# Performance work log

Hardware: AMD Instinct MI355X
Metric: run time of the kernel (lower is better)

Reference implementation:

```python
import jax, jax.numpy as jnp
import numpy as np

NUM_DIM = 1024
NUM_HEAD = 4


def setup_inputs() -> dict:
    key = jax.random.key(0)
    k1, k2, k3, k4, k5, k6 = jax.random.split(key, 6)
    B, N, C = 8, 2048, NUM_DIM
    x = jax.random.normal(k1, (B, N, C), dtype=jnp.float32)
    tmp_token = jax.random.normal(k2, (1, 1, C), dtype=jnp.float32)
    s = 1.0 / np.sqrt(C)
    Wqkv = jax.random.uniform(k3, (C, 3 * C), dtype=jnp.float32, minval=-s, maxval=s)
    bqkv = jax.random.uniform(k4, (3 * C,), dtype=jnp.float32, minval=-s, maxval=s)
    # Note: original module zero-inits v_proj; we use random weights for a
    # non-degenerate correctness baseline.
    Wv = jax.random.uniform(k5, (C, C), dtype=jnp.float32, minval=-s, maxval=s)
    bv = jax.random.uniform(k6, (C,), dtype=jnp.float32, minval=-s, maxval=s)
    return {"input": x, "tmp_token": tmp_token, "Wqkv": Wqkv, "bqkv": bqkv, "Wv": Wv, "bv": bv}


def reference(input, tmp_token, Wqkv, bqkv, Wv, bv):
    B = input.shape[0]
    # prepend learned token -> [B, N+1, C]
    x = jnp.concatenate([jnp.broadcast_to(tmp_token, (B, 1, tmp_token.shape[-1])), input], axis=1)
    B, N, C = x.shape
    H, Dh = NUM_HEAD, C // NUM_HEAD
    qkv = (x @ Wqkv + bqkv).reshape(B, N, 3, H, Dh)
    q = qkv[:, :, 0].transpose(0, 2, 1, 3)  # [B, H, N, Dh]
    k = qkv[:, :, 1].transpose(0, 2, 1, 3)
    v = qkv[:, :, 2].transpose(0, 2, 1, 3)
    scale = Dh ** (-0.5)
    scores = jnp.einsum("bhqd,bhkd->bhqk", q, k) * scale
    att = jax.nn.softmax(scores, axis=-1)  # dropout is identity in eval mode
    out = jnp.einsum("bhqk,bhkd->bhqd", att, v)
    out = out.transpose(0, 2, 1, 3).reshape(B, N, C)
    out = out @ Wv + bv  # op dropout identity in eval
    return out[:, 0, :]
```

## Files before the change

kernel.cpp:

```cpp
#include <hip/hip_runtime.h>
#include <math.h>

#define CDIM 1024
#define TC   3072
#define NIN  2048

#define OFF_Q0P 0
#define OFF_WS  16384
#define OFF_PS  20480
#define OFF_PY  24576
#define OFF_YB  2121728
#define OFF_OCP 2154496

__global__ void k_q0(const float* __restrict__ t, const float* __restrict__ W,
                     float* __restrict__ wsb) {
    int ic = blockIdx.x >> 3, jc = blockIdx.x & 7;
    int j = jc * 128 + threadIdx.x;
    int i0 = ic * 64;
    float acc = 0.f;
    for (int i = 0; i < 64; ++i)
        acc += t[i0 + i] * W[(size_t)(i0 + i) * TC + j];
    wsb[OFF_Q0P + ic * CDIM + j] = acc;
}

__global__ void k_ws(const float* __restrict__ W, const float* __restrict__ bqkv,
                     float* __restrict__ wsb) {
    int wave = threadIdx.x >> 6, lane = threadIdx.x & 63;
    int c = blockIdx.x, h = wave;
    int d0 = h * 256 + lane * 4;
    float4 wv = *(const float4*)&W[(size_t)c * TC + CDIM + d0];
    float4 q = *(const float4*)&bqkv[d0];
#pragma unroll
    for (int ic = 0; ic < 16; ++ic) {
        float4 p = *(const float4*)&wsb[OFF_Q0P + ic * CDIM + d0];
        q.x += p.x; q.y += p.y; q.z += p.z; q.w += p.w;
    }
    float acc = wv.x * q.x + wv.y * q.y + wv.z * q.z + wv.w * q.w;
    for (int off = 32; off > 0; off >>= 1) acc += __shfl_down(acc, off);
    if (lane == 0) wsb[OFF_WS + h * CDIM + c] = acc;
}

__global__ __launch_bounds__(256) void k_pass1(const float* __restrict__ x,
                                               float* __restrict__ wsb) {
    int tid = threadIdx.x, lane = tid & 63, wave = tid >> 6;
    int b = blockIdx.x >> 6, blkc = blockIdx.x & 63;

    float4 wsr[4][4];
#pragma unroll
    for (int k = 0; k < 4; ++k)
#pragma unroll
        for (int h = 0; h < 4; ++h)
            wsr[k][h] = *(const float4*)&wsb[OFF_WS + h * CDIM + k * 256 + lane * 4];

    float s[4] = {0.f, 0.f, 0.f, 0.f};
    float4 y[4][4];
#pragma unroll
    for (int h = 0; h < 4; ++h)
#pragma unroll
        for (int k = 0; k < 4; ++k) y[h][k] = make_float4(0.f, 0.f, 0.f, 0.f);

    const float* base = x + ((size_t)b * NIN + blkc * 32 + wave * 8) * CDIM;
#pragma unroll 4
    for (int i = 0; i < 8; ++i) {
        const float* row = base + (size_t)i * CDIM;
        float4 xv[4];
#pragma unroll
        for (int k = 0; k < 4; ++k) xv[k] = *(const float4*)&row[k * 256 + lane * 4];
        float e[4];
#pragma unroll
        for (int h = 0; h < 4; ++h) {
            float a = 0.f;
#pragma unroll
            for (int k = 0; k < 4; ++k)
                a += xv[k].x * wsr[k][h].x + xv[k].y * wsr[k][h].y +
                     xv[k].z * wsr[k][h].z + xv[k].w * wsr[k][h].w;
            for (int off = 1; off < 64; off <<= 1) a += __shfl_xor(a, off);
            e[h] = __expf(a * 0.0625f);
        }
#pragma unroll
        for (int h = 0; h < 4; ++h) {
            float f = e[h];
            s[h] += f;
#pragma unroll
            for (int k = 0; k < 4; ++k) {
                y[h][k].x += f * xv[k].x; y[h][k].y += f * xv[k].y;
                y[h][k].z += f * xv[k].z; y[h][k].w += f * xv[k].w;
            }
        }
    }

    __shared__ float ss[4][4];
    __shared__ float ybuf[4][CDIM];
    if (lane == 0)
#pragma unroll
        for (int h = 0; h < 4; ++h) ss[wave][h] = s[h];
    for (int idx = tid; idx < 4 * CDIM; idx += 256) ((float*)ybuf)[idx] = 0.f;
    __syncthreads();
    for (int w = 0; w < 4; ++w) {
        if (wave == w) {
#pragma unroll
            for (int h = 0; h < 4; ++h)
#pragma unroll
                for (int k = 0; k < 4; ++k) {
                    float4* dst = (float4*)&ybuf[h][k * 256 + lane * 4];
                    float4 v = *dst;
                    v.x += y[h][k].x; v.y += y[h][k].y;
                    v.z += y[h][k].z; v.w += y[h][k].w;
                    *dst = v;
                }
        }
        __syncthreads();
    }
    int p = blockIdx.x;
    if (tid < 4)
        wsb[OFF_PS + p * 4 + tid] = ss[0][tid] + ss[1][tid] + ss[2][tid] + ss[3][tid];
    for (int idx = tid; idx < 4 * CDIM; idx += 256)
        wsb[OFF_PY + (size_t)p * 4096 + idx] = ((float*)ybuf)[idx];
}

__global__ void k_comb(const float* __restrict__ t, float* __restrict__ wsb) {
    int tid = threadIdx.x, lane = tid & 63, wv = tid >> 6;
    int blk = blockIdx.x;
    int b = blk >> 4, h = (blk >> 2) & 3, cq = blk & 3;
    __shared__ float red[4], redS[4];

    int c0 = tid * 4;
    float4 tv = *(const float4*)&t[c0];
    float4 wsv = *(const float4*)&wsb[OFF_WS + h * CDIM + c0];
    float p = tv.x * wsv.x + tv.y * wsv.y + tv.z * wsv.z + tv.w * wsv.w;
    for (int off = 1; off < 64; off <<= 1) p += __shfl_xor(p, off);
    if (lane == 0) red[wv] = p;

    float sv = (tid < 64) ? wsb[OFF_PS + (size_t)(b * 64 + tid) * 4 + h] : 0.f;
    for (int off = 1; off < 64; off <<= 1) sv += __shfl_xor(sv, off);
    if (lane == 0) redS[wv] = sv;
    __syncthreads();
    float sc0 = (red[0] + red[1] + red[2] + red[3]) * 0.0625f;
    float e0 = __expf(sc0);
    float S = redS[0] + redS[1] + redS[2] + redS[3] + e0;

    int c = cq * 256 + tid;
    float acc = e0 * t[c];
#pragma unroll 4
    for (int j = 0; j < 64; ++j)
        acc += wsb[OFF_PY + (size_t)(b * 64 + j) * 4096 + h * CDIM + c];
    wsb[OFF_YB + (size_t)(b * 4 + h) * CDIM + c] = acc / S;
}

__global__ void k_ocy(const float* __restrict__ W, const float* __restrict__ bqkv,
                      float* __restrict__ wsb, float* __restrict__ out) {
    out[blockIdx.x * 128 + threadIdx.x] = 0.f;

    int p = blockIdx.x >> 3, q = blockIdx.x & 7;
    int h = p >> 1;
    __shared__ float sL[1024];
    for (int bb = 0; bb < 8; ++bb)
        sL[bb * 128 + threadIdx.x] = wsb[OFF_YB + (size_t)(bb * 4 + h) * CDIM + q * 128 + threadIdx.x];
    __syncthreads();
    int cp = p * 128 + threadIdx.x;
    float acc[8] = {0.f, 0.f, 0.f, 0.f, 0.f, 0.f, 0.f, 0.f};
    for (int c = 0; c < 128; ++c) {
        float wv = W[(size_t)(q * 128 + c) * TC + 2 * CDIM + cp];
#pragma unroll
        for (int bb = 0; bb < 8; ++bb) acc[bb] += sL[bb * 128 + c] * wv;
    }
    if (q == 0) {
        float bias = bqkv[2 * CDIM + cp];
#pragma unroll
        for (int bb = 0; bb < 8; ++bb) acc[bb] += bias;
    }
#pragma unroll
    for (int bb = 0; bb < 8; ++bb)
        wsb[OFF_OCP + (size_t)(q * 8 + bb) * CDIM + cp] = acc[bb];
}

__global__ void k_out(const float* __restrict__ Wv, const float* __restrict__ bv,
                      const float* __restrict__ wsb, float* __restrict__ out) {
    int jp = blockIdx.x >> 3, cq = blockIdx.x & 7;
    __shared__ float ocL[1024];
    for (int bb = 0; bb < 8; ++bb) {
        float sum = 0.f;
#pragma unroll
        for (int q = 0; q < 8; ++q)
            sum += wsb[OFF_OCP + (size_t)(q * 8 + bb) * CDIM + cq * 128 + threadIdx.x];
        ocL[bb * 128 + threadIdx.x] = sum;
    }
    __syncthreads();
    int j = jp * 128 + threadIdx.x;
    float acc[8] = {0.f, 0.f, 0.f, 0.f, 0.f, 0.f, 0.f, 0.f};
    for (int c = 0; c < 128; ++c) {
        float wv = Wv[(size_t)(cq * 128 + c) * CDIM + j];
#pragma unroll
        for (int bb = 0; bb < 8; ++bb) acc[bb] += ocL[bb * 128 + c] * wv;
    }
    if (cq == 0) {
        float bias = bv[j];
#pragma unroll
        for (int bb = 0; bb < 8; ++bb) acc[bb] += bias;
    }
#pragma unroll
    for (int bb = 0; bb < 8; ++bb) atomicAdd(&out[bb * CDIM + j], acc[bb]);
}

extern "C" void kernel_launch(void* const* d_in, const int* in_sizes, int n_in,
                              void* d_out, int out_size, void* d_ws, size_t ws_size,
                              hipStream_t stream) {
    const float* x    = (const float*)d_in[0];
    const float* t    = (const float*)d_in[1];
    const float* Wqkv = (const float*)d_in[2];
    const float* bqkv = (const float*)d_in[3];
    const float* Wv   = (const float*)d_in[4];
    const float* bv   = (const float*)d_in[5];
    float* wsb = (float*)d_ws;
    float* out = (float*)d_out;

    k_q0   <<<128,  128, 0, stream>>>(t, Wqkv, wsb);
    k_ws   <<<1024, 256, 0, stream>>>(Wqkv, bqkv, wsb);
    k_pass1<<<512,  256, 0, stream>>>(x, wsb);
    k_comb <<<128,  256, 0, stream>>>(t, wsb);
    k_ocy  <<<64,   128, 0, stream>>>(Wqkv, bqkv, wsb, out);
    k_out  <<<64,   128, 0, stream>>>(Wv, bv, wsb, out);
}
```

Baseline: 176.8 us.

## Fuse six kernels into one cooperative kernel with grid-wide syncs

Replaces six separate launches with one cooperative kernel of 256 blocks that separates its phases with grid.sync(). The work split is rebalanced: each block handles 64 rows of x instead of 32, which halves the partial-sum buffers. The last two GEMVs use split-K reductions in shared memory, which removes the zeroing of the output and the atomicAdd. This aims to cut launch overhead and inter-kernel gaps. The cost is grid-barrier overhead, and the x-streaming phase now runs on only 256 blocks, which may reduce memory parallelism.

```diff
diff --git a/kernel.cpp b/kernel.cpp
--- a/kernel.cpp
+++ b/kernel.cpp
@@ -1,5 +1,8 @@
 #include <hip/hip_runtime.h>
+#include <hip/hip_cooperative_groups.h>
 #include <math.h>
+
+namespace cg = cooperative_groups;
 
 #define CDIM 1024
 #define TC   3072
@@ -8,198 +11,212 @@
 #define OFF_Q0P 0
 #define OFF_WS  16384
 #define OFF_PS  20480
-#define OFF_PY  24576
-#define OFF_YB  2121728
-#define OFF_OCP 2154496
-
-__global__ void k_q0(const float* __restrict__ t, const float* __restrict__ W,
-                     float* __restrict__ wsb) {
-    int ic = blockIdx.x >> 3, jc = blockIdx.x & 7;
-    int j = jc * 128 + threadIdx.x;
-    int i0 = ic * 64;
-    float acc = 0.f;
-    for (int i = 0; i < 64; ++i)
-        acc += t[i0 + i] * W[(size_t)(i0 + i) * TC + j];
-    wsb[OFF_Q0P + ic * CDIM + j] = acc;
-}
-
-__global__ void k_ws(const float* __restrict__ W, const float* __restrict__ bqkv,
-                     float* __restrict__ wsb) {
-    int wave = threadIdx.x >> 6, lane = threadIdx.x & 63;
-    int c = blockIdx.x, h = wave;
-    int d0 = h * 256 + lane * 4;
-    float4 wv = *(const float4*)&W[(size_t)c * TC + CDIM + d0];
-    float4 q = *(const float4*)&bqkv[d0];
-#pragma unroll
-    for (int ic = 0; ic < 16; ++ic) {
-        float4 p = *(const float4*)&wsb[OFF_Q0P + ic * CDIM + d0];
-        q.x += p.x; q.y += p.y; q.z += p.z; q.w += p.w;
-    }
-    float acc = wv.x * q.x + wv.y * q.y + wv.z * q.z + wv.w * q.w;
-    for (int off = 32; off > 0; off >>= 1) acc += __shfl_down(acc, off);
-    if (lane == 0) wsb[OFF_WS + h * CDIM + c] = acc;
-}
-
-__global__ __launch_bounds__(256) void k_pass1(const float* __restrict__ x,
-                                               float* __restrict__ wsb) {
-    int tid = threadIdx.x, lane = tid & 63, wave = tid >> 6;
-    int b = blockIdx.x >> 6, blkc = blockIdx.x & 63;
-
-    float4 wsr[4][4];
-#pragma unroll
-    for (int k = 0; k < 4; ++k)
+#define OFF_PY  21504
+#define OFF_YB  1070080
+#define OFF_OC  1102848
+
+__global__ __launch_bounds__(256) void k_fused(
+    const float* __restrict__ x, const float* __restrict__ t,
+    const float* __restrict__ W, const float* __restrict__ bqkv,
+    const float* __restrict__ Wv, const float* __restrict__ bv,
+    float* __restrict__ wsb, float* __restrict__ out)
+{
+    cg::grid_group grid = cg::this_grid();
+    const int bid = blockIdx.x, tid = threadIdx.x;
+    const int lane = tid & 63, wave = tid >> 6;
+    __shared__ float lds[4112];
+
+    {
+        int ic = bid >> 4, jc = bid & 15;
+        int j = jc * 64 + lane;
+        int i0 = ic * 64 + wave * 16;
+        float acc = 0.f;
+#pragma unroll
+        for (int ii = 0; ii < 16; ++ii)
+            acc += t[i0 + ii] * W[(size_t)(i0 + ii) * TC + j];
+        lds[wave * 64 + lane] = acc;
+        __syncthreads();
+        if (wave == 0)
+            wsb[OFF_Q0P + ic * CDIM + j] =
+                lds[lane] + lds[64 + lane] + lds[128 + lane] + lds[192 + lane];
+    }
+    grid.sync();
+
+    {
+        for (int d = tid; d < CDIM; d += 256) {
+            float s = bqkv[d];
+#pragma unroll
+            for (int ic = 0; ic < 16; ++ic) s += wsb[OFF_Q0P + ic * CDIM + d];
+            lds[d] = s;
+        }
+        __syncthreads();
+        int c = bid * 4 + wave;
+        const float* wr = &W[(size_t)c * TC + CDIM];
+#pragma unroll
+        for (int h = 0; h < 4; ++h) {
+            float4 wv = *(const float4*)&wr[h * 256 + lane * 4];
+            float4 qv = *(const float4*)&lds[h * 256 + lane * 4];
+            float a = wv.x * qv.x + wv.y * qv.y + wv.z * qv.z + wv.w * qv.w;
+            for (int off = 32; off; off >>= 1) a += __shfl_down(a, off);
+            if (lane == 0) wsb[OFF_WS + h * CDIM + c] = a;
+        }
+    }
+    grid.sync();
+
+    {
+        int b = bid >> 5, blkc = bid & 31;
+        float4 wsr[4][4];
+#pragma unroll
+        for (int k = 0; k < 4; ++k)
+#pragma unroll
+            for (int h = 0; h < 4; ++h)
+                wsr[k][h] = *(const float4*)&wsb[OFF_WS + h * CDIM + k * 256 + lane * 4];
+
+        float s[4] = {0.f, 0.f, 0.f, 0.f};
+        float4 y[4][4];
 #pragma unroll
         for (int h = 0; h < 4; ++h)
-            wsr[k][h] = *(const float4*)&wsb[OFF_WS + h * CDIM + k * 256 + lane * 4];
-
-    float s[4] = {0.f, 0.f, 0.f, 0.f};
-    float4 y[4][4];
-#pragma unroll
-    for (int h = 0; h < 4; ++h)
-#pragma unroll
-        for (int k = 0; k < 4; ++k) y[h][k] = make_float4(0.f, 0.f, 0.f, 0.f);
-
-    const float* base = x + ((size_t)b * NIN + blkc * 32 + wave * 8) * CDIM;
-#pragma unroll 4
-    for (int i = 0; i < 8; ++i) {
-        const float* row = base + (size_t)i * CDIM;
-        float4 xv[4];
-#pragma unroll
-        for (int k = 0; k < 4; ++k) xv[k] = *(const float4*)&row[k * 256 + lane * 4];
-        float e[4];
-#pragma unroll
-        for (int h = 0; h < 4; ++h) {
+#pragma unroll
+            for (int k = 0; k < 4; ++k) y[h][k] = make_float4(0.f, 0.f, 0.f, 0.f);
+
+        const float* base = x + ((size_t)b * NIN + blkc * 64 + wave * 16) * CDIM;
+#pragma unroll 4
+        for (int i = 0; i < 16; ++i) {
+            const float* row = base + (size_t)i * CDIM;
+            float4 xv[4];
+#pragma unroll
+            for (int k = 0; k < 4; ++k) xv[k] = *(const float4*)&row[k * 256 + lane * 4];
+            float e[4];
+#pragma unroll
+            for (int h = 0; h < 4; ++h) {
+                float a = 0.f;
+#pragma unroll
+                for (int k = 0; k < 4; ++k)
+                    a += xv[k].x * wsr[k][h].x + xv[k].y * wsr[k][h].y +
+                         xv[k].z * wsr[k][h].z + xv[k].w * wsr[k][h].w;
+                for (int off = 1; off < 64; off <<= 1) a += __shfl_xor(a, off);
+                e[h] = __expf(a * 0.0625f);
+            }
+#pragma unroll
+            for (int h = 0; h < 4; ++h) {
+                float f = e[h];
+                s[h] += f;
+#pragma unroll
+                for (int k = 0; k < 4; ++k) {
+                    y[h][k].x += f * xv[k].x; y[h][k].y += f * xv[k].y;
+                    y[h][k].z += f * xv[k].z; y[h][k].w += f * xv[k].w;
+                }
+            }
+        }
+
+        if (lane == 0)
+#pragma unroll
+            for (int h = 0; h < 4; ++h) lds[4096 + wave * 4 + h] = s[h];
+        for (int idx = tid; idx < 4096; idx += 256) lds[idx] = 0.f;
+        __syncthreads();
+        for (int w = 0; w < 4; ++w) {
+            if (wave == w) {
+#pragma unroll
+                for (int h = 0; h < 4; ++h)
+#pragma unroll
+                    for (int k = 0; k < 4; ++k) {
+                        float4* dst = (float4*)&lds[h * CDIM + k * 256 + lane * 4];
+                        float4 v = *dst;
+                        v.x += y[h][k].x; v.y += y[h][k].y;
+                        v.z += y[h][k].z; v.w += y[h][k].w;
+                        *dst = v;
+                    }
+            }
+            __syncthreads();
+        }
+        if (tid < 4)
+            wsb[OFF_PS + bid * 4 + tid] =
+                lds[4096 + tid] + lds[4100 + tid] + lds[4104 + tid] + lds[4108 + tid];
+        for (int idx = tid; idx < 4096; idx += 256)
+            wsb[OFF_PY + (size_t)bid * 4096 + idx] = lds[idx];
+    }
+    grid.sync();
+
+    {
+        int b = bid >> 5, r = bid & 31, h = r >> 3, cq = r & 7;
+        float4 tv = *(const float4*)&t[tid * 4];
+        float4 wv = *(const float4*)&wsb[OFF_WS + h * CDIM + tid * 4];
+        float p = tv.x * wv.x + tv.y * wv.y + tv.z * wv.z + tv.w * wv.w;
+        for (int off = 1; off < 64; off <<= 1) p += __shfl_xor(p, off);
+        float sv = 0.f;
+        if (wave == 0) {
+            sv = (lane < 32) ? wsb[OFF_PS + (size_t)(b * 32 + lane) * 4 + h] : 0.f;
+            for (int off = 1; off < 64; off <<= 1) sv += __shfl_xor(sv, off);
+        }
+        if (lane == 0) lds[4096 + wave] = p;
+        if (tid == 0) lds[4100] = sv;
+        __syncthreads();
+        float sc0 = (lds[4096] + lds[4097] + lds[4098] + lds[4099]) * 0.0625f;
+        float e0 = __expf(sc0);
+        float S = lds[4100] + e0;
+
+        int c = cq * 128 + (tid & 127), half = tid >> 7;
+        float acc = 0.f;
+#pragma unroll 4
+        for (int jj = 0; jj < 16; ++jj)
+            acc += wsb[OFF_PY + (size_t)(b * 32 + half * 16 + jj) * 4096 + h * CDIM + c];
+        lds[half * 128 + (tid & 127)] = acc;
+        __syncthreads();
+        if (half == 0) {
+            float tot = lds[tid] + lds[128 + tid] + e0 * t[c];
+            wsb[OFF_YB + ((size_t)b * 4 + h) * CDIM + c] = tot / S;
+        }
+    }
+    grid.sync();
+
+    {
+        int b = bid & 7, jc = bid >> 3;
+        int hh = jc >> 3;
+        for (int d = tid; d < CDIM; d += 256)
+            lds[d] = wsb[OFF_YB + ((size_t)b * 4 + hh) * CDIM + d];
+        __syncthreads();
+        int cp = jc * 32 + (tid & 31), cs = tid >> 5;
+        const float* wcol = &W[2 * CDIM + cp];
+        float acc = 0.f;
+#pragma unroll 4
+        for (int cc = 0; cc < 128; ++cc) {
+            int c = cs * 128 + cc;
+            acc += lds[c] * wcol[(size_t)c * TC];
+        }
+        __syncthreads();
+        lds[cs * 32 + (tid & 31)] = acc;
+        __syncthreads();
+        if (cs == 0) {
             float a = 0.f;
 #pragma unroll
-            for (int k = 0; k < 4; ++k)
-                a += xv[k].x * wsr[k][h].x + xv[k].y * wsr[k][h].y +
-                     xv[k].z * wsr[k][h].z + xv[k].w * wsr[k][h].w;
-            for (int off = 1; off < 64; off <<= 1) a += __shfl_xor(a, off);
-            e[h] = __expf(a * 0.0625f);
-        }
-#pragma unroll
-        for (int h = 0; h < 4; ++h) {
-            float f = e[h];
-            s[h] += f;
-#pragma unroll
-            for (int k = 0; k < 4; ++k) {
-                y[h][k].x += f * xv[k].x; y[h][k].y += f * xv[k].y;
-                y[h][k].z += f * xv[k].z; y[h][k].w += f * xv[k].w;
-            }
-        }
-    }
-
-    __shared__ float ss[4][4];
-    __shared__ float ybuf[4][CDIM];
-    if (lane == 0)
-#pragma unroll
-        for (int h = 0; h < 4; ++h) ss[wave][h] = s[h];
-    for (int idx = tid; idx < 4 * CDIM; idx += 256) ((float*)ybuf)[idx] = 0.f;
-    __syncthreads();
-    for (int w = 0; w < 4; ++w) {
-        if (wave == w) {
-#pragma unroll
-            for (int h = 0; h < 4; ++h)
-#pragma unroll
-                for (int k = 0; k < 4; ++k) {
-                    float4* dst = (float4*)&ybuf[h][k * 256 + lane * 4];
-                    float4 v = *dst;
-                    v.x += y[h][k].x; v.y += y[h][k].y;
-                    v.z += y[h][k].z; v.w += y[h][k].w;
-                    *dst = v;
-                }
-        }
-        __syncthreads();
-    }
-    int p = blockIdx.x;
-    if (tid < 4)
-        wsb[OFF_PS + p * 4 + tid] = ss[0][tid] + ss[1][tid] + ss[2][tid] + ss[3][tid];
-    for (int idx = tid; idx < 4 * CDIM; idx += 256)
-        wsb[OFF_PY + (size_t)p * 4096 + idx] = ((float*)ybuf)[idx];
-}
-
-__global__ void k_comb(const float* __restrict__ t, float* __restrict__ wsb) {
-    int tid = threadIdx.x, lane = tid & 63, wv = tid >> 6;
-    int blk = blockIdx.x;
-    int b = blk >> 4, h = (blk >> 2) & 3, cq = blk & 3;
-    __shared__ float red[4], redS[4];
-
-    int c0 = tid * 4;
-    float4 tv = *(const float4*)&t[c0];
-    float4 wsv = *(const float4*)&wsb[OFF_WS + h * CDIM + c0];
-    float p = tv.x * wsv.x + tv.y * wsv.y + tv.z * wsv.z + tv.w * wsv.w;
-    for (int off = 1; off < 64; off <<= 1) p += __shfl_xor(p, off);
-    if (lane == 0) red[wv] = p;
-
-    float sv = (tid < 64) ? wsb[OFF_PS + (size_t)(b * 64 + tid) * 4 + h] : 0.f;
-    for (int off = 1; off < 64; off <<= 1) sv += __shfl_xor(sv, off);
-    if (lane == 0) redS[wv] = sv;
-    __syncthreads();
-    float sc0 = (red[0] + red[1] + red[2] + red[3]) * 0.0625f;
-    float e0 = __expf(sc0);
-    float S = redS[0] + redS[1] + redS[2] + redS[3] + e0;
-
-    int c = cq * 256 + tid;
-    float acc = e0 * t[c];
-#pragma unroll 4
-    for (int j = 0; j < 64; ++j)
-        acc += wsb[OFF_PY + (size_t)(b * 64 + j) * 4096 + h * CDIM + c];
-    wsb[OFF_YB + (size_t)(b * 4 + h) * CDIM + c] = acc / S;
-}
-
-__global__ void k_ocy(const float* __restrict__ W, const float* __restrict__ bqkv,
-                      float* __restrict__ wsb, float* __restrict__ out) {
-    out[blockIdx.x * 128 + threadIdx.x] = 0.f;
-
-    int p = blockIdx.x >> 3, q = blockIdx.x & 7;
-    int h = p >> 1;
-    __shared__ float sL[1024];
-    for (int bb = 0; bb < 8; ++bb)
-        sL[bb * 128 + threadIdx.x] = wsb[OFF_YB + (size_t)(bb * 4 + h) * CDIM + q * 128 + threadIdx.x];
-    __syncthreads();
-    int cp = p * 128 + threadIdx.x;
-    float acc[8] = {0.f, 0.f, 0.f, 0.f, 0.f, 0.f, 0.f, 0.f};
-    for (int c = 0; c < 128; ++c) {
-        float wv = W[(size_t)(q * 128 + c) * TC + 2 * CDIM + cp];
-#pragma unroll
-        for (int bb = 0; bb < 8; ++bb) acc[bb] += sL[bb * 128 + c] * wv;
-    }
-    if (q == 0) {
-        float bias = bqkv[2 * CDIM + cp];
-#pragma unroll
-        for (int bb = 0; bb < 8; ++bb) acc[bb] += bias;
-    }
-#pragma unroll
-    for (int bb = 0; bb < 8; ++bb)
-        wsb[OFF_OCP + (size_t)(q * 8 + bb) * CDIM + cp] = acc[bb];
-}
-
-__global__ void k_out(const float* __restrict__ Wv, const float* __restrict__ bv,
-                      const float* __restrict__ wsb, float* __restrict__ out) {
-    int jp = blockIdx.x >> 3, cq = blockIdx.x & 7;
-    __shared__ float ocL[1024];
-    for (int bb = 0; bb < 8; ++bb) {
-        float sum = 0.f;
-#pragma unroll
-        for (int q = 0; q < 8; ++q)
-            sum += wsb[OFF_OCP + (size_t)(q * 8 + bb) * CDIM + cq * 128 + threadIdx.x];
-        ocL[bb * 128 + threadIdx.x] = sum;
-    }
-    __syncthreads();
-    int j = jp * 128 + threadIdx.x;
-    float acc[8] = {0.f, 0.f, 0.f, 0.f, 0.f, 0.f, 0.f, 0.f};
-    for (int c = 0; c < 128; ++c) {
-        float wv = Wv[(size_t)(cq * 128 + c) * CDIM + j];
-#pragma unroll
-        for (int bb = 0; bb < 8; ++bb) acc[bb] += ocL[bb * 128 + c] * wv;
-    }
-    if (cq == 0) {
-        float bias = bv[j];
-#pragma unroll
-        for (int bb = 0; bb < 8; ++bb) acc[bb] += bias;
-    }
-#pragma unroll
-    for (int bb = 0; bb < 8; ++bb) atomicAdd(&out[bb * CDIM + j], acc[bb]);
+            for (int s8 = 0; s8 < 8; ++s8) a += lds[s8 * 32 + (tid & 31)];
+            wsb[OFF_OC + (size_t)b * CDIM + cp] = a + bqkv[2 * CDIM + cp];
+        }
+    }
+    grid.sync();
+
+    {
+        int b = bid & 7, jc = bid >> 3;
+        for (int d = tid; d < CDIM; d += 256)
+            lds[d] = wsb[OFF_OC + (size_t)b * CDIM + d];
+        __syncthreads();
+        int j = jc * 32 + (tid & 31), cs = tid >> 5;
+        float acc = 0.f;
+#pragma unroll 4
+        for (int cc = 0; cc < 128; ++cc) {
+            int c = cs * 128 + cc;
+            acc += lds[c] * Wv[(size_t)c * CDIM + j];
+        }
+        __syncthreads();
+        lds[cs * 32 + (tid & 31)] = acc;
+        __syncthreads();
+        if (cs == 0) {
+            float a = 0.f;
+#pragma unroll
+            for (int s8 = 0; s8 < 8; ++s8) a += lds[s8 * 32 + (tid & 31)];
+            out[(size_t)b * CDIM + j] = a + bv[j];
+        }
+    }
 }
 
 extern "C" void kernel_launch(void* const* d_in, const int* in_sizes, int n_in,
@@ -207,17 +224,15 @@
                               hipStream_t stream) {
     const float* x    = (const float*)d_in[0];
     const float* t    = (const float*)d_in[1];
-    const float* Wqkv = (const float*)d_in[2];
+    const float* W    = (const float*)d_in[2];
     const float* bqkv = (const float*)d_in[3];
     const float* Wv   = (const float*)d_in[4];
     const float* bv   = (const float*)d_in[5];
     float* wsb = (float*)d_ws;
     float* out = (float*)d_out;
 
-    k_q0   <<<128,  128, 0, stream>>>(t, Wqkv, wsb);
-    k_ws   <<<1024, 256, 0, stream>>>(Wqkv, bqkv, wsb);
-    k_pass1<<<512,  256, 0, stream>>>(x, wsb);
-    k_comb <<<128,  256, 0, stream>>>(t, wsb);
-    k_ocy  <<<64,   128, 0, stream>>>(Wqkv, bqkv, wsb, out);
-    k_out  <<<64,   128, 0, stream>>>(Wv, bv, wsb, out);
+    void* args[] = {(void*)&x, (void*)&t, (void*)&W, (void*)&bqkv,
+                    (void*)&Wv, (void*)&bv, (void*)&wsb, (void*)&out};
+    hipLaunchCooperativeKernel(reinterpret_cast<void*>(k_fused),
+                               dim3(256), dim3(256), args, 0, stream);
 }
```

Result: slower. 315.3 us (+78.3%).
